# Kernel optimization log

Measured on AMD Instinct MI355X. Metric: run time of the kernel, lower is better.

## Reference

```python
import jax, jax.numpy as jnp
import numpy as np

B, S, E = 256, 500, 128
NUM_Q, NUM_C, DL = 10000, 1000, 100


def _linear_params(key, fan_in, fan_out):
    kw, kb = jax.random.split(key)
    W = jax.random.normal(kw, (fan_out, fan_in), jnp.float32) * 0.02
    b = jnp.zeros((fan_out,), jnp.float32)
    return W, b


def setup_inputs() -> dict:
    key = jax.random.key(0)
    ks = jax.random.split(key, 24)
    W1, b1 = _linear_params(ks[0], 4 * E, E)
    W2, b2 = _linear_params(ks[1], E, E)
    W3, b3 = _linear_params(ks[2], E, E)
    W4, b4 = _linear_params(ks[3], 2 * E, E)
    W5, b5 = _linear_params(ks[4], 2 * E, E)
    W6, b6 = _linear_params(ks[5], 4 * E, E)
    inp = {
        'q': jax.random.randint(ks[6], (B, S), 0, NUM_Q + 1, dtype=jnp.int32),
        'c': jax.random.randint(ks[7], (B, S), 0, NUM_C + 1, dtype=jnp.int32),
        'sd': jax.random.randint(ks[8], (B, S), 0, DL + 2, dtype=jnp.int32),
        'qd': jax.random.randint(ks[9], (B, S), 0, DL + 2, dtype=jnp.int32),
        'a': jax.random.randint(ks[10], (B, S), 0, 2, dtype=jnp.int32),
        'qshft': jax.random.randint(ks[11], (B, S), 0, NUM_Q + 1, dtype=jnp.int32),
        'cshft': jax.random.randint(ks[12], (B, S), 0, NUM_C + 1, dtype=jnp.int32),
        'sdshft': jax.random.randint(ks[13], (B, S), 0, DL + 2, dtype=jnp.int32),
        'qdshft': jax.random.randint(ks[14], (B, S), 0, DL + 2, dtype=jnp.int32),
        'q_embedding': jax.random.normal(ks[15], (B, S, E), jnp.float32),
        'c_tab': jax.random.normal(ks[16], (NUM_C + 1, E), jnp.float32) * 0.02,
        'sd_tab': jax.random.normal(ks[17], (DL + 2, E), jnp.float32) * 0.02,
        'qd_tab': jax.random.normal(ks[18], (DL + 2, E), jnp.float32) * 0.02,
        'a_tab': jax.random.normal(ks[19], (2, E), jnp.float32) * 0.02,
        'knowledge': jax.random.normal(ks[20], (1, E), jnp.float32) * 0.1,
        'W1': W1, 'b1': b1, 'W2': W2, 'b2': b2, 'W3': W3, 'b3': b3,
        'W4': W4, 'b4': b4, 'W5': W5, 'b5': b5, 'W6': W6, 'b6': b6,
    }
    return inp


def reference(q, c, sd, qd, a, qshft, cshft, sdshft, qdshft, q_embedding,
              c_tab, sd_tab, qd_tab, a_tab, knowledge,
              W1, b1, W2, b2, W3, b3, W4, b4, W5, b5, W6, b6):
    # padding_idx=0 embeddings -> zero row 0
    mask0 = lambda t: t.at[0].set(0.0)
    c_e = mask0(c_tab)[c]      # [B,S,E]
    sd_e = mask0(sd_tab)[sd]   # [B,S,E]
    qd_e = mask0(qd_tab)[qd]   # [B,S,E]
    a_e = a_tab[a]             # [B,S,E]
    # linear_1 on concatenated (q, c, sd, qd) embeddings
    input_data = jnp.concatenate([q_embedding, c_e, sd_e, qd_e], -1) @ W1.T + b1  # [B,S,E]
    # time-major for scan
    xs = (jnp.swapaxes(input_data, 0, 1), jnp.swapaxes(a_e, 0, 1),
          jnp.swapaxes(sd_e, 0, 1), jnp.swapaxes(qd_e, 0, 1))
    k0 = jnp.broadcast_to(knowledge, (q.shape[0], knowledge.shape[1]))  # [B,E]

    def step(k, x):
        inp_t, a_t, sd_t, qd_t = x
        qq = k - inp_t
        g_sdf = jax.nn.sigmoid(qq @ W2.T + b2)
        sdft = g_sdf * jnp.tanh(qq @ W3.T + b3)      # dropout in eval mode = identity
        xcat = jnp.concatenate([sdft, a_t], -1)
        g_pka = jax.nn.sigmoid(xcat @ W4.T + b4)
        pkat = g_pka * jnp.tanh(xcat @ W5.T + b5)
        ins = jnp.concatenate([k, a_t, sd_t, qd_t], -1)
        g_ksu = jax.nn.sigmoid(ins @ W6.T + b6)
        k_new = g_ksu * k + (1.0 - g_ksu) * pkat
        return k_new, None

    k_final, _ = jax.lax.scan(step, k0, xs)
    return jax.nn.sigmoid(k_final)  # [B,E]
```

## Files before the change

kernel.cpp:

```cpp
#include <hip/hip_runtime.h>

typedef unsigned short u16;
typedef unsigned int u32;
typedef short bf16x8 __attribute__((ext_vector_type(8)));
typedef float f32x4 __attribute__((ext_vector_type(4)));

#define S_LEN 500
#define NB 256
#define EDIM 128

__device__ __forceinline__ float bf2f(u16 u) { return __uint_as_float(((u32)u) << 16); }
__device__ __forceinline__ u16 f2bf(float f) {
    u32 x = __float_as_uint(f);
    x += 0x7FFFu + ((x >> 16) & 1u);
    return (u16)(x >> 16);
}
__device__ __forceinline__ u32 cvtpk(float lo, float hi) {
    u32 r;
    asm("v_cvt_pk_bf16_f32 %0, %1, %2" : "=v"(r) : "v"(lo), "v"(hi));
    return r;
}
__device__ __forceinline__ float fexp(float x) { return __builtin_amdgcn_exp2f(x * 1.44269504089f); }
__device__ __forceinline__ float frcp(float x) { return __builtin_amdgcn_rcpf(x); }
__device__ __forceinline__ float sigm(float x) { return frcp(1.0f + fexp(-x)); }
__device__ __forceinline__ float tanh_(float x) { return 1.0f - 2.0f * frcp(1.0f + fexp(2.0f * x)); }
__device__ __forceinline__ int iclamp(int v, int hi) { return v < 0 ? 0 : (v > hi ? hi : v); }

__device__ __forceinline__ void wgsync(volatile int* c, int target) {
    __asm__ volatile("s_waitcnt lgkmcnt(0)" ::: "memory");
    if ((threadIdx.x & 63) == 0) atomicAdd((int*)c, 1);
    while (*c < target) {}
    __asm__ volatile("" ::: "memory");
}

__device__ __forceinline__ bool detect_bf16(const void* q) {
    const u16* w = (const u16*)q;
    int plaus = 0;
#pragma unroll 1
    for (int i = 0; i < 64; ++i) {
        const u16 v = w[2 * i];
        const int e = (v >> 7) & 0xFF;
        plaus += (v == 0 || (e >= 100 && e <= 130)) ? 1 : 0;
    }
    return plaus >= 48;
}
__device__ __forceinline__ float ldF(const void* p, int i, bool bf) {
    return bf ? bf2f(((const u16*)p)[i]) : ((const float*)p)[i];
}
template <bool BF>
__device__ __forceinline__ bf16x8 ldfragT(const void* p, int i) {
    if (BF) return *(const bf16x8*)((const u16*)p + i);
    const float* f = (const float*)p + i;
    bf16x8 r;
#pragma unroll
    for (int e = 0; e < 8; ++e) r[e] = (short)f2bf(f[e]);
    return r;
}
__device__ __forceinline__ bf16x8 ldfragR(const void* p, int i, bool bf) {
    if (bf) return *(const bf16x8*)((const u16*)p + i);
    const float* f = (const float*)p + i;
    bf16x8 r;
#pragma unroll
    for (int e = 0; e < 8; ++e) r[e] = (short)f2bf(f[e]);
    return r;
}

__global__ void dimkt_sentinel(u16* __restrict__ out, u16 val) {
    out[blockIdx.x * 256 + threadIdx.x] = val;
}

__global__ void dimkt_tabs(const void* __restrict__ q_emb,
                           const void* __restrict__ c_tab, const void* __restrict__ sd_tab,
                           const void* __restrict__ qd_tab, const void* __restrict__ a_tab,
                           const void* __restrict__ W1, const void* __restrict__ W4,
                           const void* __restrict__ W5, const void* __restrict__ W6,
                           const void* __restrict__ b4, const void* __restrict__ b5,
                           const void* __restrict__ b6,
                           float* __restrict__ cW1p, float* __restrict__ sdQ,
                           float* __restrict__ qdQ, float* __restrict__ aW6p,
                           float* __restrict__ c4t, float* __restrict__ c5t) {
    const bool bf = detect_bf16(q_emb);
    __shared__ float src[128];
    const int r = blockIdx.x, n = threadIdx.x;
    const void* srcp; const void* W; const void* bias = nullptr;
    int soff, koff, ld, oidx; float* outp; bool mask;
    if (r < 1001)      { srcp = c_tab;  soff = r * 128;               W = W1; koff = 128; ld = 512; outp = cW1p; oidx = r * 128 + n;           mask = (r == 0); }
    else if (r < 1103) { int rr = r - 1001; srcp = sd_tab; soff = rr * 128; W = W1; koff = 256; ld = 512; outp = sdQ;  oidx = rr * 256 + n * 2;     mask = (rr == 0); }
    else if (r < 1205) { int rr = r - 1103; srcp = qd_tab; soff = rr * 128; W = W1; koff = 384; ld = 512; outp = qdQ;  oidx = rr * 256 + n * 2;     mask = (rr == 0); }
    else if (r < 1307) { int rr = r - 1205; srcp = sd_tab; soff = rr * 128; W = W6; koff = 256; ld = 512; outp = sdQ;  oidx = rr * 256 + n * 2 + 1; mask = (rr == 0); }
    else if (r < 1409) { int rr = r - 1307; srcp = qd_tab; soff = rr * 128; W = W6; koff = 384; ld = 512; outp = qdQ;  oidx = rr * 256 + n * 2 + 1; mask = (rr == 0); }
    else if (r < 1411) { int rr = r - 1409; srcp = a_tab;  soff = rr * 128; W = W6; koff = 128; ld = 512; outp = aW6p; oidx = rr * 128 + n;         bias = b6; mask = false; }
    else if (r < 1413) { int rr = r - 1411; srcp = a_tab;  soff = rr * 128; W = W4; koff = 128; ld = 256; outp = c4t;  oidx = rr * 128 + n;         bias = b4; mask = false; }
    else               { int rr = r - 1413; srcp = a_tab;  soff = rr * 128; W = W5; koff = 128; ld = 256; outp = c5t;  oidx = rr * 128 + n;         bias = b5; mask = false; }
    src[n] = ldF(srcp, soff + n, bf);
    __syncthreads();
    float acc = 0.f;
    if (!mask) {
        if (bf) {
            const u16* Wp = (const u16*)W + n * ld + koff;
#pragma unroll 4
            for (int k = 0; k < 128; k += 8) {
                const ushort4 wa = *(const ushort4*)(Wp + k);
                const ushort4 wb = *(const ushort4*)(Wp + k + 4);
                acc += src[k] * bf2f(wa.x) + src[k + 1] * bf2f(wa.y)
                     + src[k + 2] * bf2f(wa.z) + src[k + 3] * bf2f(wa.w)
                     + src[k + 4] * bf2f(wb.x) + src[k + 5] * bf2f(wb.y)
                     + src[k + 6] * bf2f(wb.z) + src[k + 7] * bf2f(wb.w);
            }
        } else {
            const float* Wp = (const float*)W + n * ld + koff;
#pragma unroll 4
            for (int k = 0; k < 128; k += 4) {
                const float4 w4 = *(const float4*)(Wp + k);
                acc += src[k] * w4.x + src[k + 1] * w4.y + src[k + 2] * w4.z + src[k + 3] * w4.w;
            }
        }
        if (bias) acc += ldF(bias, n, bf);
    }
    outp[oidx] = acc;
}

__global__ void dimkt_inp(const void* __restrict__ q_emb,
                          const void* __restrict__ W1, const void* __restrict__ b1,
                          const int* __restrict__ cI, const int* __restrict__ sI,
                          const int* __restrict__ qI,
                          const float* __restrict__ cW1p, const float* __restrict__ sdQ,
                          const float* __restrict__ qdQ, u16* __restrict__ INP16) {
    const bool bf = detect_bf16(q_emb);
    const int t = blockIdx.x, rc = blockIdx.y;
    const int lane = threadIdx.x, quad = lane >> 4, l15 = lane & 15;
    bf16x8 ae[4];
#pragma unroll
    for (int ks = 0; ks < 4; ++ks)
        ae[ks] = ldfragR(q_emb, ((rc * 16 + l15) * S_LEN + t) * EDIM + ks * 32 + quad * 8, bf);
    int cx[4], sx[4], qx[4];
#pragma unroll
    for (int i = 0; i < 4; ++i) {
        const int off = (rc * 16 + quad * 4 + i) * S_LEN + t;
        cx[i] = iclamp(cI[off], 1000);
        sx[i] = iclamp(sI[off], 101);
        qx[i] = iclamp(qI[off], 101);
    }
#pragma unroll 1
    for (int ct = 0; ct < 8; ++ct) {
        const int col = ct * 16 + l15;
        bf16x8 w[4];
#pragma unroll
        for (int ks = 0; ks < 4; ++ks)
            w[ks] = ldfragR(W1, col * 512 + ks * 32 + quad * 8, bf);
        const float b1c = ldF(b1, col, bf);
        f32x4 acc;
#pragma unroll
        for (int i = 0; i < 4; ++i)
            acc[i] = b1c + cW1p[cx[i] * 128 + col]
                   + sdQ[sx[i] * 256 + col * 2] + qdQ[qx[i] * 256 + col * 2];
#pragma unroll
        for (int ks = 0; ks < 4; ++ks)
            acc = __builtin_amdgcn_mfma_f32_16x16x32_bf16(ae[ks], w[ks], acc, 0, 0, 0);
#pragma unroll
        for (int i = 0; i < 4; ++i)
            INP16[(t * 256 + rc * 16 + quad * 4 + i) * 128 + col] = f2bf(acc[i]);
    }
}

template <bool BF>
__global__ __launch_bounds__(512, 2) void dimkt_scan(
    const void* __restrict__ q_emb, const u16* __restrict__ INP16,
    const int* __restrict__ cI, const int* __restrict__ sI,
    const int* __restrict__ qI, const int* __restrict__ aI,
    const void* __restrict__ W2, const void* __restrict__ b2,
    const void* __restrict__ W3, const void* __restrict__ b3,
    const void* __restrict__ W4, const void* __restrict__ W5,
    const void* __restrict__ W6, const void* __restrict__ knowledge,
    const float* __restrict__ sdQ, const float* __restrict__ qdQ,
    const float* __restrict__ aW6p, const float* __restrict__ c4t,
    const float* __restrict__ c5t, void* __restrict__ outv) {
    if (detect_bf16(q_emb) != BF) return;
    __shared__ __align__(16) u16 kbuf[16][136];
    __shared__ __align__(16) u16 qqbuf[16][136];
    __shared__ __align__(16) u16 sdbuf[16][136];
    __shared__ u32 idxL[16][S_LEN];
    __shared__ int sctr;
    extern __shared__ __align__(16) u16 dynLDS[];
    u16* sdT = dynLDS;
    u16* qdT = dynLDS + 102 * 130;
    float* aW6L = (float*)(dynLDS + 2 * 102 * 130);

    const int tid = threadIdx.x;
    const int wv = tid >> 6, lane = tid & 63;
    const int quad = lane >> 4, l15 = lane & 15;
    const int b0 = blockIdx.x * 16;
    const int col = wv * 16 + l15;
    const int col2 = col * 2;

    bf16x8 fW2[4], fW3[4], fW4[4], fW5[4], fW6[4];
#pragma unroll
    for (int ks = 0; ks < 4; ++ks) {
        const int ko = ks * 32 + quad * 8;
        fW2[ks] = ldfragT<BF>(W2, col * 128 + ko);
        fW3[ks] = ldfragT<BF>(W3, col * 128 + ko);
        fW4[ks] = ldfragT<BF>(W4, col * 256 + ko);
        fW5[ks] = ldfragT<BF>(W5, col * 256 + ko);
        fW6[ks] = ldfragT<BF>(W6, col * 512 + ko);
    }
    const float b2v = ldF(b2, col, BF);
    const float b3v = ldF(b3, col, BF);
    const float c4_0 = c4t[col], c4_1 = c4t[128 + col];
    const float c5_0 = c5t[col], c5_1 = c5t[128 + col];

#pragma unroll 1
    for (int r = 0; r < 16; ++r)
#pragma unroll 1
        for (int t = tid; t < S_LEN; t += 512) {
            const int off = (b0 + r) * S_LEN + t;
            idxL[r][t] = (u32)iclamp(cI[off], 1000)
                       | ((u32)iclamp(sI[off], 101) << 10)
                       | ((u32)iclamp(qI[off], 101) << 17)
                       | ((u32)iclamp(aI[off], 1) << 24);
        }

#pragma unroll 1
    for (int v = tid; v < 102 * 128; v += 512) {
        const int sx = v >> 7, cc = v & 127;
        sdT[sx * 130 + cc] = f2bf(sdQ[sx * 256 + cc * 2 + 1]);
        qdT[sx * 130 + cc] = f2bf(qdQ[sx * 256 + cc * 2 + 1]);
    }
    if (tid < 256) {
        const int rr = tid >> 7, cc = tid & 127;
        aW6L[rr * 132 + cc] = aW6p[rr * 128 + cc];
    }
    if (tid == 0) sctr = 0;
    __syncthreads();

    float kold[4], z6c[4], g[4];
    int ac[4];
    {
        const float k0 = ldF(knowledge, col, BF);
        const u16 k0b = f2bf(k0);
#pragma unroll
        for (int i = 0; i < 4; ++i) {
            const u32 p = idxL[quad * 4 + i][0];
            const int sx = (p >> 10) & 127, qx = (p >> 17) & 127, ax = (p >> 24) & 1;
            ac[i] = ax;
            const float2 sgp = *(const float2*)(sdQ + sx * 256 + col2);
            const float2 qgp = *(const float2*)(qdQ + qx * 256 + col2);
            z6c[i] = aW6p[ax * 128 + col] + sgp.y + qgp.y;
            const float inp0 = bf2f(INP16[(0 * 256 + b0 + quad * 4 + i) * 128 + col]);
            kold[i] = k0;
            kbuf[quad * 4 + i][col] = k0b;
            qqbuf[quad * 4 + i][col] = f2bf(k0 - inp0);
        }
    }
    u32 pk4[4];
#pragma unroll
    for (int i = 0; i < 4; ++i) pk4[i] = idxL[quad * 4 + i][1];

    __syncthreads();

    int bar = 0;
#pragma unroll 1
    for (int t = 0; t < S_LEN; ++t) {
        const int tf2 = (t + 2 < S_LEN) ? t + 2 : S_LEN - 1;
        const int tp = (t + 1 < S_LEN) ? t + 1 : S_LEN - 1;
        int an[4];
        u16 inpN[4];
        float sw6[4], qw6[4], agv[4];
#pragma unroll
        for (int i = 0; i < 4; ++i) {
            const u32 p = pk4[i];
            const int sx = (p >> 10) & 127, qx = (p >> 17) & 127;
            an[i] = (p >> 24) & 1;
            inpN[i] = INP16[(tp * 256 + b0 + quad * 4 + i) * 128 + col];
            sw6[i] = bf2f(sdT[sx * 130 + col]);
            qw6[i] = bf2f(qdT[qx * 130 + col]);
            agv[i] = aW6L[an[i] * 132 + col];
        }
#pragma unroll
        for (int i = 0; i < 4; ++i) pk4[i] = idxL[quad * 4 + i][tf2];

        bf16x8 aq[4], ak[4];
#pragma unroll
        for (int ks = 0; ks < 4; ++ks) {
            aq[ks] = *(const bf16x8*)&qqbuf[l15][ks * 32 + quad * 8];
            ak[ks] = *(const bf16x8*)&kbuf[l15][ks * 32 + quad * 8];
        }
        f32x4 Y2a = (f32x4){b2v, b2v, b2v, b2v}, Y2b = (f32x4){0.f, 0.f, 0.f, 0.f};
        f32x4 Y3a = (f32x4){b3v, b3v, b3v, b3v}, Y3b = (f32x4){0.f, 0.f, 0.f, 0.f};
        f32x4 Y6a = (f32x4){z6c[0], z6c[1], z6c[2], z6c[3]}, Y6b = (f32x4){0.f, 0.f, 0.f, 0.f};
        Y2a = __builtin_amdgcn_mfma_f32_16x16x32_bf16(aq[0], fW2[0], Y2a, 0, 0, 0);
        Y3a = __builtin_amdgcn_mfma_f32_16x16x32_bf16(aq[0], fW3[0], Y3a, 0, 0, 0);
        Y6a = __builtin_amdgcn_mfma_f32_16x16x32_bf16(ak[0], fW6[0], Y6a, 0, 0, 0);
        Y2b = __builtin_amdgcn_mfma_f32_16x16x32_bf16(aq[2], fW2[2], Y2b, 0, 0, 0);
        Y3b = __builtin_amdgcn_mfma_f32_16x16x32_bf16(aq[2], fW3[2], Y3b, 0, 0, 0);
        Y6b = __builtin_amdgcn_mfma_f32_16x16x32_bf16(ak[2], fW6[2], Y6b, 0, 0, 0);
        Y2a = __builtin_amdgcn_mfma_f32_16x16x32_bf16(aq[1], fW2[1], Y2a, 0, 0, 0);
        Y3a = __builtin_amdgcn_mfma_f32_16x16x32_bf16(aq[1], fW3[1], Y3a, 0, 0, 0);
        Y6a = __builtin_amdgcn_mfma_f32_16x16x32_bf16(ak[1], fW6[1], Y6a, 0, 0, 0);
        Y2b = __builtin_amdgcn_mfma_f32_16x16x32_bf16(aq[3], fW2[3], Y2b, 0, 0, 0);
        Y3b = __builtin_amdgcn_mfma_f32_16x16x32_bf16(aq[3], fW3[3], Y3b, 0, 0, 0);
        Y6b = __builtin_amdgcn_mfma_f32_16x16x32_bf16(ak[3], fW6[3], Y6b, 0, 0, 0);
        f32x4 Y2 = Y2a + Y2b, Y3 = Y3a + Y3b, Y6 = Y6a + Y6b;
        float sdv[4];
#pragma unroll
        for (int i = 0; i < 4; ++i) sdv[i] = sigm(Y2[i]) * tanh_(Y3[i]);
        {
            const u32 s01 = cvtpk(sdv[0], sdv[1]), s23 = cvtpk(sdv[2], sdv[3]);
            sdbuf[quad * 4 + 0][col] = (u16)s01;
            sdbuf[quad * 4 + 1][col] = (u16)(s01 >> 16);
            sdbuf[quad * 4 + 2][col] = (u16)s23;
            sdbuf[quad * 4 + 3][col] = (u16)(s23 >> 16);
        }
        bar += 8; wgsync(&sctr, bar);

        bf16x8 as[4];
#pragma unroll
        for (int ks = 0; ks < 4; ++ks)
            as[ks] = *(const bf16x8*)&sdbuf[l15][ks * 32 + quad * 8];
#pragma unroll
        for (int i = 0; i < 4; ++i) g[i] = sigm(Y6[i]);
        f32x4 Y4a = (f32x4){ac[0] ? c4_1 : c4_0, ac[1] ? c4_1 : c4_0,
                            ac[2] ? c4_1 : c4_0, ac[3] ? c4_1 : c4_0};
        f32x4 Y5a = (f32x4){ac[0] ? c5_1 : c5_0, ac[1] ? c5_1 : c5_0,
                            ac[2] ? c5_1 : c5_0, ac[3] ? c5_1 : c5_0};
        f32x4 Y4b = (f32x4){0.f, 0.f, 0.f, 0.f}, Y5b = (f32x4){0.f, 0.f, 0.f, 0.f};
        Y4a = __builtin_amdgcn_mfma_f32_16x16x32_bf16(as[0], fW4[0], Y4a, 0, 0, 0);
        Y5a = __builtin_amdgcn_mfma_f32_16x16x32_bf16(as[0], fW5[0], Y5a, 0, 0, 0);
        Y4b = __builtin_amdgcn_mfma_f32_16x16x32_bf16(as[2], fW4[2], Y4b, 0, 0, 0);
        Y5b = __builtin_amdgcn_mfma_f32_16x16x32_bf16(as[2], fW5[2], Y5b, 0, 0, 0);
        Y4a = __builtin_amdgcn_mfma_f32_16x16x32_bf16(as[1], fW4[1], Y4a, 0, 0, 0);
        Y5a = __builtin_amdgcn_mfma_f32_16x16x32_bf16(as[1], fW5[1], Y5a, 0, 0, 0);
        Y4b = __builtin_amdgcn_mfma_f32_16x16x32_bf16(as[3], fW4[3], Y4b, 0, 0, 0);
        Y5b = __builtin_amdgcn_mfma_f32_16x16x32_bf16(as[3], fW5[3], Y5b, 0, 0, 0);
        const f32x4 Y4 = Y4a + Y4b, Y5 = Y5a + Y5b;
        float knA[4], qqA[4];
#pragma unroll
        for (int i = 0; i < 4; ++i) {
            const float pk = sigm(Y4[i]) * tanh_(Y5[i]);
            const float kn = g[i] * kold[i] + (1.0f - g[i]) * pk;
            kold[i] = kn; knA[i] = kn;
            qqA[i] = kn - bf2f(inpN[i]);
        }
        {
            const u32 k01 = cvtpk(knA[0], knA[1]), k23 = cvtpk(knA[2], knA[3]);
            const u32 q01 = cvtpk(qqA[0], qqA[1]), q23 = cvtpk(qqA[2], qqA[3]);
            kbuf[quad * 4 + 0][col] = (u16)k01;
            kbuf[quad * 4 + 1][col] = (u16)(k01 >> 16);
            kbuf[quad * 4 + 2][col] = (u16)k23;
            kbuf[quad * 4 + 3][col] = (u16)(k23 >> 16);
            qqbuf[quad * 4 + 0][col] = (u16)q01;
            qqbuf[quad * 4 + 1][col] = (u16)(q01 >> 16);
            qqbuf[quad * 4 + 2][col] = (u16)q23;
            qqbuf[quad * 4 + 3][col] = (u16)(q23 >> 16);
        }
#pragma unroll
        for (int i = 0; i < 4; ++i) {
            z6c[i] = agv[i] + sw6[i] + qw6[i];
            ac[i] = an[i];
        }
        bar += 8; wgsync(&sctr, bar);
    }

#pragma unroll
    for (int i = 0; i < 4; ++i) {
        const int row = quad * 4 + i;
        const float v = sigm(kold[i]);
        const int off = (b0 + row) * EDIM + col;
        if (BF) ((u16*)outv)[off] = f2bf(v);
        else    ((float*)outv)[off] = v;
    }
}

extern "C" void kernel_launch(void* const* d_in, const int* in_sizes, int n_in,
                              void* d_out, int out_size, void* d_ws, size_t ws_size,
                              hipStream_t stream) {
    static const int exp_sizes[27] = {
        128000, 128000, 128000, 128000, 128000,
        128000, 128000, 128000, 128000,
        16384000,
        128128, 13056, 13056, 256, 128,
        65536, 128, 16384, 128, 16384, 128,
        32768, 128, 32768, 128, 65536, 128
    };
    bool sizes_ok = (n_in == 27) && (out_size == 32768);
    if (sizes_ok)
        for (int i = 0; i < 27; ++i)
            if (in_sizes[i] != exp_sizes[i]) { sizes_ok = false; break; }
    if (!sizes_ok) {
        dimkt_sentinel<<<dim3(128), dim3(256), 0, stream>>>((u16*)d_out, (u16)0xC080);
        return;
    }
    const size_t WS_NEED = 724480;
    const size_t WS_NEED16 = WS_NEED + 32768000u;
    if (ws_size < WS_NEED16) {
        dimkt_sentinel<<<dim3(128), dim3(256), 0, stream>>>((u16*)d_out, (u16)0x4110);
        return;
    }

    const int* c   = (const int*)d_in[1];
    const int* sd  = (const int*)d_in[2];
    const int* qd  = (const int*)d_in[3];
    const int* a   = (const int*)d_in[4];
    const void* q_emb = d_in[9];
    const void* c_tab = d_in[10];
    const void* sd_tab = d_in[11];
    const void* qd_tab = d_in[12];
    const void* a_tab = d_in[13];
    const void* knowledge = d_in[14];
    const void* W1 = d_in[15]; const void* b1 = d_in[16];
    const void* W2 = d_in[17]; const void* b2 = d_in[18];
    const void* W3 = d_in[19]; const void* b3 = d_in[20];
    const void* W4 = d_in[21]; const void* b4 = d_in[22];
    const void* W5 = d_in[23]; const void* b5 = d_in[24];
    const void* W6 = d_in[25]; const void* b6 = d_in[26];

    float* wsf = (float*)d_ws;
    float* cW1p = wsf;
    float* sdQ  = wsf + 128128;
    float* qdQ  = wsf + 154240;
    float* aW6p = wsf + 180352;
    float* c4t  = wsf + 180608;
    float* c5t  = wsf + 180864;
    u16* INP16  = (u16*)((char*)d_ws + WS_NEED);

    constexpr int DYN_BYTES = 2 * 102 * 130 * 2 + 2 * 132 * 4;
    hipFuncSetAttribute(reinterpret_cast<const void*>(&dimkt_scan<true>),
                        hipFuncAttributeMaxDynamicSharedMemorySize, DYN_BYTES);
    hipFuncSetAttribute(reinterpret_cast<const void*>(&dimkt_scan<false>),
                        hipFuncAttributeMaxDynamicSharedMemorySize, DYN_BYTES);

    dimkt_tabs<<<dim3(1415), dim3(128), 0, stream>>>(
        q_emb, c_tab, sd_tab, qd_tab, a_tab, W1, W4, W5, W6, b4, b5, b6,
        cW1p, sdQ, qdQ, aW6p, c4t, c5t);

    dimkt_inp<<<dim3(500, 16), dim3(64), 0, stream>>>(
        q_emb, W1, b1, c, sd, qd, cW1p, sdQ, qdQ, INP16);

    dimkt_scan<true><<<dim3(16), dim3(512), DYN_BYTES, stream>>>(
        q_emb, INP16, c, sd, qd, a, W2, b2, W3, b3, W4, W5, W6, knowledge,
        sdQ, qdQ, aW6p, c4t, c5t, d_out);
    dimkt_scan<false><<<dim3(16), dim3(512), DYN_BYTES, stream>>>(
        q_emb, INP16, c, sd, qd, a, W2, b2, W3, b3, W4, W5, W6, knowledge,
        sdQ, qdQ, aW6p, c4t, c5t, d_out);
}
```

Before: 1.030 ms.

## Precompute packed input and W6 gate terms in transposed layout for the scan

The input-projection kernel now also computes the a/sd/qd contribution to the W6 gate and packs it with the linear_1 output as a bf16 pair. It writes the pair into a time-major, column-major buffer so the serial scan loads one uint4 per step instead of gathering from LDS tables and index arrays. This drops the scan's index preload and the sd/qd table staging in LDS. A separate path pre-converts q_embedding and W1 to bf16 when the workspace is large enough. Which path runs depends on the workspace size, and the packed buffer needs twice the workspace.

```diff
diff --git a/kernel.cpp b/kernel.cpp
--- a/kernel.cpp
+++ b/kernel.cpp
@@ -67,6 +67,25 @@
 
 __global__ void dimkt_sentinel(u16* __restrict__ out, u16 val) {
     out[blockIdx.x * 256 + threadIdx.x] = val;
+}
+
+__global__ void dimkt_qe16(const float* __restrict__ qf, u16* __restrict__ qe16) {
+    if (detect_bf16(qf)) return;
+    const int i = (blockIdx.x * 256 + threadIdx.x) * 8;
+    const float4 a = *(const float4*)(qf + i);
+    const float4 b = *(const float4*)(qf + i + 4);
+    ushort4 lo, hi;
+    lo.x = f2bf(a.x); lo.y = f2bf(a.y); lo.z = f2bf(a.z); lo.w = f2bf(a.w);
+    hi.x = f2bf(b.x); hi.y = f2bf(b.y); hi.z = f2bf(b.z); hi.w = f2bf(b.w);
+    *(ushort4*)(qe16 + i) = lo;
+    *(ushort4*)(qe16 + i + 4) = hi;
+}
+
+__global__ void dimkt_w1bf(const void* __restrict__ W1, const void* __restrict__ qref,
+                           u16* __restrict__ W1b) {
+    const bool bf = detect_bf16(qref);
+    const int i = blockIdx.x * 256 + threadIdx.x;
+    W1b[i] = bf ? ((const u16*)W1)[i] : f2bf(((const float*)W1)[i]);
 }
 
 __global__ void dimkt_tabs(const void* __restrict__ q_emb,
@@ -120,51 +139,232 @@
     outp[oidx] = acc;
 }
 
-__global__ void dimkt_inp(const void* __restrict__ q_emb,
+__global__ void dimkt_inp(const void* __restrict__ q_emb, const u16* __restrict__ qe16,
+                          const u16* __restrict__ W1b, const int fastpath,
                           const void* __restrict__ W1, const void* __restrict__ b1,
                           const int* __restrict__ cI, const int* __restrict__ sI,
-                          const int* __restrict__ qI,
+                          const int* __restrict__ qI, const int* __restrict__ aI,
                           const float* __restrict__ cW1p, const float* __restrict__ sdQ,
-                          const float* __restrict__ qdQ, u16* __restrict__ INP16) {
+                          const float* __restrict__ qdQ, const float* __restrict__ aW6p,
+                          u16* __restrict__ INP16, u32* __restrict__ INPZ6T, const int pk) {
     const bool bf = detect_bf16(q_emb);
     const int t = blockIdx.x, rc = blockIdx.y;
     const int lane = threadIdx.x, quad = lane >> 4, l15 = lane & 15;
+    const bool fA = bf || (fastpath != 0);
+    const u16* aes = bf ? (const u16*)q_emb : qe16;
     bf16x8 ae[4];
 #pragma unroll
-    for (int ks = 0; ks < 4; ++ks)
-        ae[ks] = ldfragR(q_emb, ((rc * 16 + l15) * S_LEN + t) * EDIM + ks * 32 + quad * 8, bf);
-    int cx[4], sx[4], qx[4];
+    for (int ks = 0; ks < 4; ++ks) {
+        const int off = ((rc * 16 + l15) * S_LEN + t) * EDIM + ks * 32 + quad * 8;
+        ae[ks] = fA ? *(const bf16x8*)(aes + off) : ldfragR(q_emb, off, false);
+    }
+    int cx[4], sx[4], qx[4], ax[4];
 #pragma unroll
     for (int i = 0; i < 4; ++i) {
         const int off = (rc * 16 + quad * 4 + i) * S_LEN + t;
         cx[i] = iclamp(cI[off], 1000);
         sx[i] = iclamp(sI[off], 101);
         qx[i] = iclamp(qI[off], 101);
+        ax[i] = iclamp(aI[off], 1);
     }
 #pragma unroll 1
     for (int ct = 0; ct < 8; ++ct) {
-        const int col = ct * 16 + l15;
+        const int colc = ct * 16 + l15;
         bf16x8 w[4];
 #pragma unroll
-        for (int ks = 0; ks < 4; ++ks)
-            w[ks] = ldfragR(W1, col * 512 + ks * 32 + quad * 8, bf);
-        const float b1c = ldF(b1, col, bf);
-        f32x4 acc;
-#pragma unroll
-        for (int i = 0; i < 4; ++i)
-            acc[i] = b1c + cW1p[cx[i] * 128 + col]
-                   + sdQ[sx[i] * 256 + col * 2] + qdQ[qx[i] * 256 + col * 2];
+        for (int ks = 0; ks < 4; ++ks) {
+            const int woff = colc * 512 + ks * 32 + quad * 8;
+            w[ks] = fastpath ? *(const bf16x8*)(W1b + woff) : ldfragR(W1, woff, bf);
+        }
+        const float b1c = ldF(b1, colc, bf);
+        f32x4 acc; float z6v[4];
+#pragma unroll
+        for (int i = 0; i < 4; ++i) {
+            const float2 sgp = *(const float2*)(sdQ + sx[i] * 256 + colc * 2);
+            const float2 qgp = *(const float2*)(qdQ + qx[i] * 256 + colc * 2);
+            acc[i] = b1c + cW1p[cx[i] * 128 + colc] + sgp.x + qgp.x;
+            z6v[i] = pk ? (aW6p[ax[i] * 128 + colc] + sgp.y + qgp.y) : 0.f;
+        }
 #pragma unroll
         for (int ks = 0; ks < 4; ++ks)
             acc = __builtin_amdgcn_mfma_f32_16x16x32_bf16(ae[ks], w[ks], acc, 0, 0, 0);
-#pragma unroll
-        for (int i = 0; i < 4; ++i)
-            INP16[(t * 256 + rc * 16 + quad * 4 + i) * 128 + col] = f2bf(acc[i]);
+        if (pk) {
+            uint4 st;
+            st.x = cvtpk(acc[0], z6v[0]); st.y = cvtpk(acc[1], z6v[1]);
+            st.z = cvtpk(acc[2], z6v[2]); st.w = cvtpk(acc[3], z6v[3]);
+            *(uint4*)(INPZ6T + ((size_t)t * 128 + colc) * 256 + rc * 16 + quad * 4) = st;
+        } else {
+#pragma unroll
+            for (int i = 0; i < 4; ++i)
+                INP16[((size_t)t * 256 + rc * 16 + quad * 4 + i) * 128 + colc] = f2bf(acc[i]);
+        }
     }
 }
 
 template <bool BF>
-__global__ __launch_bounds__(512, 2) void dimkt_scan(
+__global__ __launch_bounds__(512, 2) void dimkt_scan_pk(
+    const void* __restrict__ q_emb, const u32* __restrict__ INPZ6T,
+    const int* __restrict__ aI,
+    const void* __restrict__ W2, const void* __restrict__ b2,
+    const void* __restrict__ W3, const void* __restrict__ b3,
+    const void* __restrict__ W4, const void* __restrict__ W5,
+    const void* __restrict__ W6, const void* __restrict__ knowledge,
+    const float* __restrict__ c4t, const float* __restrict__ c5t,
+    void* __restrict__ outv) {
+    if (detect_bf16(q_emb) != BF) return;
+    __shared__ __align__(16) u16 kbuf[16][136];
+    __shared__ __align__(16) u16 qqbuf[16][136];
+    __shared__ __align__(16) u16 sdbuf[16][136];
+    __shared__ int sctr;
+
+    const int tid = threadIdx.x;
+    const int wv = tid >> 6, lane = tid & 63;
+    const int quad = lane >> 4, l15 = lane & 15;
+    const int b0 = blockIdx.x * 16;
+    const int col = wv * 16 + l15;
+
+    bf16x8 fW2[4], fW3[4], fW4[4], fW5[4], fW6[4];
+#pragma unroll
+    for (int ks = 0; ks < 4; ++ks) {
+        const int ko = ks * 32 + quad * 8;
+        fW2[ks] = ldfragT<BF>(W2, col * 128 + ko);
+        fW3[ks] = ldfragT<BF>(W3, col * 128 + ko);
+        fW4[ks] = ldfragT<BF>(W4, col * 256 + ko);
+        fW5[ks] = ldfragT<BF>(W5, col * 256 + ko);
+        fW6[ks] = ldfragT<BF>(W6, col * 512 + ko);
+    }
+    const float b2v = ldF(b2, col, BF);
+    const float b3v = ldF(b3, col, BF);
+    const float c4_0 = c4t[col], c4_1 = c4t[128 + col];
+    const float c5_0 = c5t[col], c5_1 = c5t[128 + col];
+
+    const u32* pzBase = INPZ6T + (size_t)col * 256 + b0 + quad * 4;
+    const int aRow = (b0 + quad * 4) * S_LEN;
+
+    float kold[4], z6c[4], g[4];
+    int ac[4];
+    {
+        const float k0 = ldF(knowledge, col, BF);
+        const u16 k0b = f2bf(k0);
+        const uint4 pz0 = *(const uint4*)pzBase;
+        const u32 pzv[4] = {pz0.x, pz0.y, pz0.z, pz0.w};
+        if (tid == 0) sctr = 0;
+#pragma unroll
+        for (int i = 0; i < 4; ++i) {
+            ac[i] = iclamp(aI[aRow + i * S_LEN], 1);
+            z6c[i] = __uint_as_float(pzv[i] & 0xFFFF0000u);
+            const float inp0 = __uint_as_float(pzv[i] << 16);
+            kold[i] = k0;
+            kbuf[quad * 4 + i][col] = k0b;
+            qqbuf[quad * 4 + i][col] = f2bf(k0 - inp0);
+        }
+    }
+    __syncthreads();
+
+    int bar = 0;
+#pragma unroll 1
+    for (int t = 0; t < S_LEN; ++t) {
+        const int tp = (t + 1 < S_LEN) ? t + 1 : S_LEN - 1;
+        int an[4];
+#pragma unroll
+        for (int i = 0; i < 4; ++i) an[i] = iclamp(aI[aRow + i * S_LEN + tp], 1);
+        const uint4 pzN = *(const uint4*)(pzBase + (size_t)tp * 32768);
+
+        bf16x8 aq[4], ak[4];
+#pragma unroll
+        for (int ks = 0; ks < 4; ++ks) {
+            aq[ks] = *(const bf16x8*)&qqbuf[l15][ks * 32 + quad * 8];
+            ak[ks] = *(const bf16x8*)&kbuf[l15][ks * 32 + quad * 8];
+        }
+        f32x4 Y2a = (f32x4){b2v, b2v, b2v, b2v}, Y2b = (f32x4){0.f, 0.f, 0.f, 0.f};
+        f32x4 Y3a = (f32x4){b3v, b3v, b3v, b3v}, Y3b = (f32x4){0.f, 0.f, 0.f, 0.f};
+        f32x4 Y6a = (f32x4){z6c[0], z6c[1], z6c[2], z6c[3]}, Y6b = (f32x4){0.f, 0.f, 0.f, 0.f};
+        Y2a = __builtin_amdgcn_mfma_f32_16x16x32_bf16(aq[0], fW2[0], Y2a, 0, 0, 0);
+        Y3a = __builtin_amdgcn_mfma_f32_16x16x32_bf16(aq[0], fW3[0], Y3a, 0, 0, 0);
+        Y6a = __builtin_amdgcn_mfma_f32_16x16x32_bf16(ak[0], fW6[0], Y6a, 0, 0, 0);
+        Y2b = __builtin_amdgcn_mfma_f32_16x16x32_bf16(aq[2], fW2[2], Y2b, 0, 0, 0);
+        Y3b = __builtin_amdgcn_mfma_f32_16x16x32_bf16(aq[2], fW3[2], Y3b, 0, 0, 0);
+        Y6b = __builtin_amdgcn_mfma_f32_16x16x32_bf16(ak[2], fW6[2], Y6b, 0, 0, 0);
+        Y2a = __builtin_amdgcn_mfma_f32_16x16x32_bf16(aq[1], fW2[1], Y2a, 0, 0, 0);
+        Y3a = __builtin_amdgcn_mfma_f32_16x16x32_bf16(aq[1], fW3[1], Y3a, 0, 0, 0);
+        Y6a = __builtin_amdgcn_mfma_f32_16x16x32_bf16(ak[1], fW6[1], Y6a, 0, 0, 0);
+        Y2b = __builtin_amdgcn_mfma_f32_16x16x32_bf16(aq[3], fW2[3], Y2b, 0, 0, 0);
+        Y3b = __builtin_amdgcn_mfma_f32_16x16x32_bf16(aq[3], fW3[3], Y3b, 0, 0, 0);
+        Y6b = __builtin_amdgcn_mfma_f32_16x16x32_bf16(ak[3], fW6[3], Y6b, 0, 0, 0);
+        const f32x4 Y2 = Y2a + Y2b, Y3 = Y3a + Y3b, Y6 = Y6a + Y6b;
+        float sdv[4];
+#pragma unroll
+        for (int i = 0; i < 4; ++i) sdv[i] = sigm(Y2[i]) * tanh_(Y3[i]);
+        {
+            const u32 s01 = cvtpk(sdv[0], sdv[1]), s23 = cvtpk(sdv[2], sdv[3]);
+            sdbuf[quad * 4 + 0][col] = (u16)s01;
+            sdbuf[quad * 4 + 1][col] = (u16)(s01 >> 16);
+            sdbuf[quad * 4 + 2][col] = (u16)s23;
+            sdbuf[quad * 4 + 3][col] = (u16)(s23 >> 16);
+        }
+        bar += 8; wgsync(&sctr, bar);
+
+        bf16x8 as[4];
+#pragma unroll
+        for (int ks = 0; ks < 4; ++ks)
+            as[ks] = *(const bf16x8*)&sdbuf[l15][ks * 32 + quad * 8];
+#pragma unroll
+        for (int i = 0; i < 4; ++i) g[i] = sigm(Y6[i]);
+        f32x4 Y4a = (f32x4){ac[0] ? c4_1 : c4_0, ac[1] ? c4_1 : c4_0,
+                            ac[2] ? c4_1 : c4_0, ac[3] ? c4_1 : c4_0};
+        f32x4 Y5a = (f32x4){ac[0] ? c5_1 : c5_0, ac[1] ? c5_1 : c5_0,
+                            ac[2] ? c5_1 : c5_0, ac[3] ? c5_1 : c5_0};
+        f32x4 Y4b = (f32x4){0.f, 0.f, 0.f, 0.f}, Y5b = (f32x4){0.f, 0.f, 0.f, 0.f};
+        Y4a = __builtin_amdgcn_mfma_f32_16x16x32_bf16(as[0], fW4[0], Y4a, 0, 0, 0);
+        Y5a = __builtin_amdgcn_mfma_f32_16x16x32_bf16(as[0], fW5[0], Y5a, 0, 0, 0);
+        Y4b = __builtin_amdgcn_mfma_f32_16x16x32_bf16(as[2], fW4[2], Y4b, 0, 0, 0);
+        Y5b = __builtin_amdgcn_mfma_f32_16x16x32_bf16(as[2], fW5[2], Y5b, 0, 0, 0);
+        Y4a = __builtin_amdgcn_mfma_f32_16x16x32_bf16(as[1], fW4[1], Y4a, 0, 0, 0);
+        Y5a = __builtin_amdgcn_mfma_f32_16x16x32_bf16(as[1], fW5[1], Y5a, 0, 0, 0);
+        Y4b = __builtin_amdgcn_mfma_f32_16x16x32_bf16(as[3], fW4[3], Y4b, 0, 0, 0);
+        Y5b = __builtin_amdgcn_mfma_f32_16x16x32_bf16(as[3], fW5[3], Y5b, 0, 0, 0);
+        const f32x4 Y4 = Y4a + Y4b, Y5 = Y5a + Y5b;
+        const u32 pzv[4] = {pzN.x, pzN.y, pzN.z, pzN.w};
+        float knA[4], qqA[4];
+#pragma unroll
+        for (int i = 0; i < 4; ++i) {
+            const float pk = sigm(Y4[i]) * tanh_(Y5[i]);
+            const float kn = g[i] * kold[i] + (1.0f - g[i]) * pk;
+            kold[i] = kn; knA[i] = kn;
+            qqA[i] = kn - __uint_as_float(pzv[i] << 16);
+        }
+        {
+            const u32 k01 = cvtpk(knA[0], knA[1]), k23 = cvtpk(knA[2], knA[3]);
+            const u32 q01 = cvtpk(qqA[0], qqA[1]), q23 = cvtpk(qqA[2], qqA[3]);
+            kbuf[quad * 4 + 0][col] = (u16)k01;
+            kbuf[quad * 4 + 1][col] = (u16)(k01 >> 16);
+            kbuf[quad * 4 + 2][col] = (u16)k23;
+            kbuf[quad * 4 + 3][col] = (u16)(k23 >> 16);
+            qqbuf[quad * 4 + 0][col] = (u16)q01;
+            qqbuf[quad * 4 + 1][col] = (u16)(q01 >> 16);
+            qqbuf[quad * 4 + 2][col] = (u16)q23;
+            qqbuf[quad * 4 + 3][col] = (u16)(q23 >> 16);
+        }
+#pragma unroll
+        for (int i = 0; i < 4; ++i) {
+            z6c[i] = __uint_as_float(pzv[i] & 0xFFFF0000u);
+            ac[i] = an[i];
+        }
+        bar += 8; wgsync(&sctr, bar);
+    }
+
+#pragma unroll
+    for (int i = 0; i < 4; ++i) {
+        const int row = quad * 4 + i;
+        const float v = sigm(kold[i]);
+        const int off = (b0 + row) * EDIM + col;
+        if (BF) ((u16*)outv)[off] = f2bf(v);
+        else    ((float*)outv)[off] = v;
+    }
+}
+
+template <bool BF>
+__global__ __launch_bounds__(512, 2) void dimkt_scan_fb(
     const void* __restrict__ q_emb, const u16* __restrict__ INP16,
     const int* __restrict__ cI, const int* __restrict__ sI,
     const int* __restrict__ qI, const int* __restrict__ aI,
@@ -218,7 +418,6 @@
                        | ((u32)iclamp(qI[off], 101) << 17)
                        | ((u32)iclamp(aI[off], 1) << 24);
         }
-
 #pragma unroll 1
     for (int v = tid; v < 102 * 128; v += 512) {
         const int sx = v >> 7, cc = v & 127;
@@ -245,7 +444,7 @@
             const float2 sgp = *(const float2*)(sdQ + sx * 256 + col2);
             const float2 qgp = *(const float2*)(qdQ + qx * 256 + col2);
             z6c[i] = aW6p[ax * 128 + col] + sgp.y + qgp.y;
-            const float inp0 = bf2f(INP16[(0 * 256 + b0 + quad * 4 + i) * 128 + col]);
+            const float inp0 = bf2f(INP16[(size_t)(b0 + quad * 4 + i) * 128 + col]);
             kold[i] = k0;
             kbuf[quad * 4 + i][col] = k0b;
             qqbuf[quad * 4 + i][col] = f2bf(k0 - inp0);
@@ -254,7 +453,6 @@
     u32 pk4[4];
 #pragma unroll
     for (int i = 0; i < 4; ++i) pk4[i] = idxL[quad * 4 + i][1];
-
     __syncthreads();
 
     int bar = 0;
@@ -270,7 +468,7 @@
             const u32 p = pk4[i];
             const int sx = (p >> 10) & 127, qx = (p >> 17) & 127;
             an[i] = (p >> 24) & 1;
-            inpN[i] = INP16[(tp * 256 + b0 + quad * 4 + i) * 128 + col];
+            inpN[i] = INP16[((size_t)tp * 256 + b0 + quad * 4 + i) * 128 + col];
             sw6[i] = bf2f(sdT[sx * 130 + col]);
             qw6[i] = bf2f(qdT[qx * 130 + col]);
             agv[i] = aW6L[an[i] * 132 + col];
@@ -299,7 +497,7 @@
         Y2b = __builtin_amdgcn_mfma_f32_16x16x32_bf16(aq[3], fW2[3], Y2b, 0, 0, 0);
         Y3b = __builtin_amdgcn_mfma_f32_16x16x32_bf16(aq[3], fW3[3], Y3b, 0, 0, 0);
         Y6b = __builtin_amdgcn_mfma_f32_16x16x32_bf16(ak[3], fW6[3], Y6b, 0, 0, 0);
-        f32x4 Y2 = Y2a + Y2b, Y3 = Y3a + Y3b, Y6 = Y6a + Y6b;
+        const f32x4 Y2 = Y2a + Y2b, Y3 = Y3a + Y3b, Y6 = Y6a + Y6b;
         float sdv[4];
 #pragma unroll
         for (int i = 0; i < 4; ++i) sdv[i] = sigm(Y2[i]) * tanh_(Y3[i]);
@@ -390,11 +588,15 @@
         return;
     }
     const size_t WS_NEED = 724480;
-    const size_t WS_NEED16 = WS_NEED + 32768000u;
-    if (ws_size < WS_NEED16) {
+    const size_t WS_FB   = WS_NEED + 32768000u;
+    if (ws_size < WS_FB) {
         dimkt_sentinel<<<dim3(128), dim3(256), 0, stream>>>((u16*)d_out, (u16)0x4110);
         return;
     }
+    const size_t WS_PK   = WS_NEED + 65536000u;
+    const size_t WS_FAST = WS_PK + 32768000u + 131072u;
+    const int pk   = (ws_size >= WS_PK) ? 1 : 0;
+    const int fast = (ws_size >= WS_FAST) ? 1 : 0;
 
     const int* c   = (const int*)d_in[1];
     const int* sd  = (const int*)d_in[2];
@@ -421,24 +623,39 @@
     float* c4t  = wsf + 180608;
     float* c5t  = wsf + 180864;
     u16* INP16  = (u16*)((char*)d_ws + WS_NEED);
-
-    constexpr int DYN_BYTES = 2 * 102 * 130 * 2 + 2 * 132 * 4;
-    hipFuncSetAttribute(reinterpret_cast<const void*>(&dimkt_scan<true>),
-                        hipFuncAttributeMaxDynamicSharedMemorySize, DYN_BYTES);
-    hipFuncSetAttribute(reinterpret_cast<const void*>(&dimkt_scan<false>),
-                        hipFuncAttributeMaxDynamicSharedMemorySize, DYN_BYTES);
+    u32* INPZ6T = (u32*)((char*)d_ws + WS_NEED);
+    u16* qe16   = (u16*)((char*)d_ws + WS_PK);
+    u16* W1b    = (u16*)((char*)d_ws + WS_PK + 32768000u);
 
     dimkt_tabs<<<dim3(1415), dim3(128), 0, stream>>>(
         q_emb, c_tab, sd_tab, qd_tab, a_tab, W1, W4, W5, W6, b4, b5, b6,
         cW1p, sdQ, qdQ, aW6p, c4t, c5t);
 
+    if (fast) {
+        dimkt_qe16<<<dim3(8000), dim3(256), 0, stream>>>((const float*)q_emb, qe16);
+        dimkt_w1bf<<<dim3(256), dim3(256), 0, stream>>>(W1, q_emb, W1b);
+    }
+
     dimkt_inp<<<dim3(500, 16), dim3(64), 0, stream>>>(
-        q_emb, W1, b1, c, sd, qd, cW1p, sdQ, qdQ, INP16);
-
-    dimkt_scan<true><<<dim3(16), dim3(512), DYN_BYTES, stream>>>(
-        q_emb, INP16, c, sd, qd, a, W2, b2, W3, b3, W4, W5, W6, knowledge,
-        sdQ, qdQ, aW6p, c4t, c5t, d_out);
-    dimkt_scan<false><<<dim3(16), dim3(512), DYN_BYTES, stream>>>(
-        q_emb, INP16, c, sd, qd, a, W2, b2, W3, b3, W4, W5, W6, knowledge,
-        sdQ, qdQ, aW6p, c4t, c5t, d_out);
-}
+        q_emb, qe16, W1b, fast, W1, b1, c, sd, qd, a,
+        cW1p, sdQ, qdQ, aW6p, INP16, INPZ6T, pk);
+
+    if (pk) {
+        dimkt_scan_pk<true><<<dim3(16), dim3(512), 0, stream>>>(
+            q_emb, INPZ6T, a, W2, b2, W3, b3, W4, W5, W6, knowledge, c4t, c5t, d_out);
+        dimkt_scan_pk<false><<<dim3(16), dim3(512), 0, stream>>>(
+            q_emb, INPZ6T, a, W2, b2, W3, b3, W4, W5, W6, knowledge, c4t, c5t, d_out);
+    } else {
+        constexpr int DYN_BYTES = 2 * 102 * 130 * 2 + 2 * 132 * 4;
+        hipFuncSetAttribute(reinterpret_cast<const void*>(&dimkt_scan_fb<true>),
+                            hipFuncAttributeMaxDynamicSharedMemorySize, DYN_BYTES);
+        hipFuncSetAttribute(reinterpret_cast<const void*>(&dimkt_scan_fb<false>),
+                            hipFuncAttributeMaxDynamicSharedMemorySize, DYN_BYTES);
+        dimkt_scan_fb<true><<<dim3(16), dim3(512), DYN_BYTES, stream>>>(
+            q_emb, INP16, c, sd, qd, a, W2, b2, W3, b3, W4, W5, W6, knowledge,
+            sdQ, qdQ, aW6p, c4t, c5t, d_out);
+        dimkt_scan_fb<false><<<dim3(16), dim3(512), DYN_BYTES, stream>>>(
+            q_emb, INP16, c, sd, qd, a, W2, b2, W3, b3, W4, W5, W6, knowledge,
+            sdQ, qdQ, aW6p, c4t, c5t, d_out);
+    }
+}
```

Measured after the change: 998.3 us. 3.1% less time.
